# Kernel optimization log

Measured on AMD Instinct MI355X. Metric: run time of the kernel, lower is better.

Reference implementation:

```python
import jax, jax.numpy as jnp
import numpy as np

N_HEADS = 16
KEY_DIM = 64
VAL_DIM = 64
HIDDEN = 1024
SCALE = 1.0 / float(KEY_DIM) ** 0.5


def setup_inputs() -> dict:
    key = jax.random.key(0)
    ks = jax.random.split(key, 16)
    B, Lq, Lk, R = 2, 2048, 2048, 2048
    inp = {
        "query": jax.random.normal(ks[0], (B, Lq, HIDDEN), jnp.float32),
        "value": jax.random.normal(ks[1], (B, Lk, HIDDEN), jnp.float32),
        "positional_embedding": jax.random.normal(ks[2], (R, HIDDEN), jnp.float32),
        "u_weight": jax.random.normal(ks[3], (N_HEADS, KEY_DIM), jnp.float32) * 0.02,
        "v_weight": jax.random.normal(ks[4], (N_HEADS, KEY_DIM), jnp.float32) * 0.02,
        "indices": jax.random.randint(ks[5], (2, Lq, Lk), 0, R, jnp.int64 if jax.config.jax_enable_x64 else jnp.int32),
        "lower": jax.random.uniform(ks[6], (Lq, Lk), jnp.float32),
    }
    s = 0.02
    inp["Wq"] = jax.random.normal(ks[7], (HIDDEN, N_HEADS * KEY_DIM), jnp.float32) * s
    inp["bq"] = jnp.zeros((N_HEADS * KEY_DIM,), jnp.float32)
    inp["Wk"] = jax.random.normal(ks[8], (HIDDEN, N_HEADS * KEY_DIM), jnp.float32) * s
    inp["bk"] = jnp.zeros((N_HEADS * KEY_DIM,), jnp.float32)
    inp["Wv"] = jax.random.normal(ks[9], (HIDDEN, N_HEADS * VAL_DIM), jnp.float32) * s
    inp["bv"] = jnp.zeros((N_HEADS * VAL_DIM,), jnp.float32)
    inp["Wr"] = jax.random.normal(ks[10], (HIDDEN, N_HEADS * KEY_DIM), jnp.float32) * s
    inp["br"] = jnp.zeros((N_HEADS * KEY_DIM,), jnp.float32)
    inp["Wo"] = jax.random.normal(ks[11], (N_HEADS * VAL_DIM, HIDDEN), jnp.float32) * s
    inp["bo"] = jnp.zeros((HIDDEN,), jnp.float32)
    return inp


def reference(query, value, positional_embedding, u_weight, v_weight, indices, lower,
              Wq, bq, Wk, bk, Wv, bv, Wr, br, Wo, bo):
    B, Lq, _ = query.shape
    Lk = value.shape[1]
    R = positional_embedding.shape[0]
    # projections (torch Linear with weights stored as [in, out])
    q = (query @ Wq + bq).reshape(B, Lq, N_HEADS, KEY_DIM)
    k = (value @ Wk + bk).reshape(B, Lk, N_HEADS, KEY_DIM)
    v = (value @ Wv + bv).reshape(B, Lk, N_HEADS, VAL_DIM)
    r = (positional_embedding @ Wr + br).reshape(R, N_HEADS, KEY_DIM)
    # content (AC) and position (BD) score terms -> [i, j, b, n]
    AC = jnp.einsum("bind,bjnd->ijbn", q + u_weight, k)
    BD = jnp.einsum("bind,jnd->ijbn", q + v_weight, r)
    # rel-shift: gather [Lq, R] -> [Lq, Lk] positions, then apply lower mask
    BD = BD[indices[0], indices[1]] * lower[:, :, None, None]
    attn = jax.nn.softmax((AC + BD) * SCALE, axis=1)  # softmax over key dim j
    out = jnp.einsum("ijbn,bjnd->bind", attn, v).reshape(B, Lq, N_HEADS * VAL_DIM)
    return out @ Wo + bo
```

## Files before the change

kernel.cpp:

```cpp
#include <hip/hip_runtime.h>
#include <stdint.h>

typedef __attribute__((ext_vector_type(8))) short short8;
typedef __attribute__((ext_vector_type(4))) float f32x4;
typedef unsigned short u16;
typedef unsigned int u32;
typedef unsigned long long u64;

#define LQ 2048
#define LK 2048
#define RDIM 2048
#define HID 1024
#define NH 16
#define DH 64
#define S2SCALE 0.1803368801111204f

__device__ __forceinline__ float bf2f(u16 u){
  union { unsigned int i; float f; } v; v.i = ((unsigned int)u) << 16; return v.f;
}
__device__ __forceinline__ u16 f2bf(float f){
  union { float f; unsigned int i; } v; v.f = f;
  unsigned int r = v.i + 0x7fffu + ((v.i >> 16) & 1u);
  return (u16)(r >> 16);
}
__device__ __forceinline__ f32x4 fzero(){ f32x4 z = {0.0f, 0.0f, 0.0f, 0.0f}; return z; }

__global__ void k_detect(const u32* __restrict__ q, const u32* __restrict__ idxw,
                         int* __restrict__ flags){
  int t = threadIdx.x;
  u32 w = q[t];
  int b = (w >> 7) & 0xFF;
  unsigned long long mb = __ballot(b >= 100 && b <= 140);
  u32 hi = idxw[2 * t + 1];
  unsigned long long mi = __ballot(hi == 0u);
  if (t == 0){
    flags[0] = (__popcll(mb) >= 48) ? 1 : 0;
    flags[1] = (__popcll(mi) == 64) ? 1 : 0;
  }
}

struct Seg { const void* src; u16* dst; int n4; };
struct SegPack { Seg s[8]; };
__global__ void k_ingestN(SegPack p, const int* __restrict__ flags){
  int f = flags[0];
  Seg sg = p.s[blockIdx.y];
  int stride = gridDim.x * blockDim.x;
  for (int i = blockIdx.x * blockDim.x + threadIdx.x; i < sg.n4; i += stride){
    if (f){
      reinterpret_cast<uint2*>(sg.dst)[i] = reinterpret_cast<const uint2*>(sg.src)[i];
    } else {
      float4 v = reinterpret_cast<const float4*>(sg.src)[i];
      union { u16 h[4]; uint2 u; } t;
      t.h[0] = f2bf(v.x); t.h[1] = f2bf(v.y); t.h[2] = f2bf(v.z); t.h[3] = f2bf(v.w);
      reinterpret_cast<uint2*>(sg.dst)[i] = t.u;
    }
  }
}

struct WPack { const void* src[5]; u16* dst[5]; };
__global__ void k_wtrans(WPack p, const int* __restrict__ flags){
  int f = flags[0];
  const void* W = p.src[blockIdx.z];
  u16* Wt = p.dst[blockIdx.z];
  __shared__ u16 t[64][65];
  int tid = threadIdx.x;
  int bx = blockIdx.x, by = blockIdx.y;
#pragma unroll
  for (int it = 0; it < 16; ++it){
    int id = it * 256 + tid;
    int r = id >> 6, c = id & 63;
    size_t so = (size_t)(by * 64 + r) * HID + bx * 64 + c;
    t[r][c] = f ? ((const u16*)W)[so] : f2bf(((const float*)W)[so]);
  }
  __syncthreads();
#pragma unroll
  for (int it = 0; it < 16; ++it){
    int id = it * 256 + tid;
    int r = id >> 6, c = id & 63;
    Wt[(size_t)(bx * 64 + r) * HID + by * 64 + c] = t[c][r];
  }
}

__global__ void k_goff(const int* __restrict__ idx, int* __restrict__ goff,
                       const int* __restrict__ flags){
  int i64f = flags[1];
  const size_t N = (size_t)LQ * LK;
  size_t stride = (size_t)gridDim.x * blockDim.x;
  for (size_t t = (size_t)blockIdx.x * blockDim.x + threadIdx.x; t < N; t += stride){
    long long a0, a1;
    if (i64f){
      const long long* ip = (const long long*)idx;
      a0 = ip[t]; a1 = ip[N + t];
    } else {
      a0 = idx[t]; a1 = idx[N + t];
    }
    goff[t] = (int)(a0 * RDIM + a1);
  }
}

__global__ void k_gemm(const u16* __restrict__ A, const u16* __restrict__ Bt,
                       const u16* __restrict__ bias,
                       const u16* __restrict__ add0, const u16* __restrict__ add1,
                       void* __restrict__ D0, u16* __restrict__ D1,
                       int headmajor, const int* __restrict__ oflags){
  __shared__ u16 As[128][72];
  __shared__ u16 Bs[128][72];
  int tid = threadIdx.x;
  int l = tid & 63, w = tid >> 6;
  int lr = l & 15, g = l >> 4;
  int wr = w >> 1, wc = w & 1;
  int outf32 = oflags ? (oflags[0] == 0) : 0;
  f32x4 acc[4][4];
#pragma unroll
  for (int a = 0; a < 4; ++a)
#pragma unroll
    for (int bq_ = 0; bq_ < 4; ++bq_) acc[a][bq_] = fzero();
  const size_t arowg = (size_t)blockIdx.x * 128;
  const size_t browg = (size_t)blockIdx.y * 128;
  for (int kt = 0; kt < HID; kt += 64){
#pragma unroll
    for (int it = 0; it < 4; ++it){
      int id = it * 256 + tid;
      int r = id >> 3, ch = id & 7;
      uint4 va = *reinterpret_cast<const uint4*>(A + (arowg + r) * HID + kt + ch * 8);
      *reinterpret_cast<uint4*>(&As[r][ch * 8]) = va;
      uint4 vb = *reinterpret_cast<const uint4*>(Bt + (browg + r) * HID + kt + ch * 8);
      *reinterpret_cast<uint4*>(&Bs[r][ch * 8]) = vb;
    }
    __syncthreads();
#pragma unroll
    for (int ks = 0; ks < 2; ++ks){
      short8 af[4], bfv[4];
#pragma unroll
      for (int mf = 0; mf < 4; ++mf)
        af[mf] = *reinterpret_cast<const short8*>(&As[wr * 64 + mf * 16 + lr][ks * 32 + 8 * g]);
#pragma unroll
      for (int nf = 0; nf < 4; ++nf)
        bfv[nf] = *reinterpret_cast<const short8*>(&Bs[wc * 64 + nf * 16 + lr][ks * 32 + 8 * g]);
#pragma unroll
      for (int mf = 0; mf < 4; ++mf)
#pragma unroll
        for (int nf = 0; nf < 4; ++nf)
          acc[mf][nf] = __builtin_amdgcn_mfma_f32_16x16x32_bf16(af[mf], bfv[nf], acc[mf][nf], 0, 0, 0);
    }
    __syncthreads();
  }
#pragma unroll
  for (int mf = 0; mf < 4; ++mf)
#pragma unroll
    for (int nf = 0; nf < 4; ++nf){
      int col = (int)browg + wc * 64 + nf * 16 + lr;
      float bcol = bf2f(bias[col]);
      float a0 = add0 ? bf2f(add0[col]) : 0.0f;
      float a1 = add1 ? bf2f(add1[col]) : 0.0f;
#pragma unroll
      for (int reg = 0; reg < 4; ++reg){
        int row = (int)arowg + wr * 64 + mf * 16 + 4 * g + reg;
        float base = acc[mf][nf][reg] + bcol;
        if (headmajor == 2){
          int b = row >> 11, i = row & 2047;
          int n32 = col >> 6, d = col & 63;
          u16* Dx = (n32 < NH) ? (u16*)D0 : D1;
          size_t dst = ((size_t)(b * NH + (n32 & (NH - 1))) * LQ + i) * DH + d;
          Dx[dst] = f2bf(base);
        } else if (headmajor == 1){
          int b = row >> 11, i = row & 2047;
          int n = col >> 6, d = col & 63;
          size_t dst = ((size_t)(b * NH + n) * LQ + i) * DH + d;
          ((u16*)D0)[dst] = f2bf(base + a0);
          if (D1) D1[dst] = f2bf(base + a1);
        } else {
          size_t dst = (size_t)row * HID + col;
          if (outf32) ((float*)D0)[dst] = base;
          else        ((u16*)D0)[dst] = f2bf(base);
        }
      }
    }
}

__global__ void k_bdfull16(const u16* __restrict__ qv, const u16* __restrict__ rr,
                           u16* __restrict__ bdf, int bnBase){
  __shared__ u16 tile[32][64][16];
  int tid = threadIdx.x;
  int l = tid & 63, w = tid >> 6;
  int lr = l & 15, g = l >> 4;
  int i0 = blockIdx.x * 32, j0 = blockIdx.y * 64;
#pragma unroll
  for (int hh = 0; hh < 4; ++hh){
    int g_ = w * 4 + hh;
    int bn = bnBase + g_;
    int b = bn >> 4, n = bn & 15;
    const u16* qb = qv + ((size_t)(b * NH + n) * LQ + i0) * DH;
    const u16* rb = rr + ((size_t)n * RDIM + j0) * DH;
    short8 af[2][2];
#pragma unroll
    for (int mf = 0; mf < 2; ++mf)
#pragma unroll
      for (int ks = 0; ks < 2; ++ks)
        af[mf][ks] = *reinterpret_cast<const short8*>(qb + (size_t)(mf * 16 + lr) * DH + ks * 32 + 8 * g);
    f32x4 acc[2][4];
#pragma unroll
    for (int mf = 0; mf < 2; ++mf)
#pragma unroll
      for (int nf = 0; nf < 4; ++nf) acc[mf][nf] = fzero();
#pragma unroll
    for (int nf = 0; nf < 4; ++nf){
#pragma unroll
      for (int ks = 0; ks < 2; ++ks){
        short8 bb = *reinterpret_cast<const short8*>(rb + (size_t)(nf * 16 + lr) * DH + ks * 32 + 8 * g);
#pragma unroll
        for (int mf = 0; mf < 2; ++mf)
          acc[mf][nf] = __builtin_amdgcn_mfma_f32_16x16x32_bf16(af[mf][ks], bb, acc[mf][nf], 0, 0, 0);
      }
    }
#pragma unroll
    for (int mf = 0; mf < 2; ++mf)
#pragma unroll
      for (int nf = 0; nf < 4; ++nf)
#pragma unroll
        for (int reg = 0; reg < 4; ++reg)
          tile[mf * 16 + 4 * g + reg][nf * 16 + lr][g_] = f2bf(acc[mf][nf][reg]);
  }
  __syncthreads();
#pragma unroll
  for (int e = 0; e < 32; ++e){
    int id = e * 256 + tid;
    int line = id >> 2, part = id & 3;
    int ii = line >> 6, jj = line & 63;
    u64 v = *reinterpret_cast<const u64*>(&tile[ii][jj][part * 4]);
    *reinterpret_cast<u64*>(
        bdf + ((size_t)(i0 + ii) * RDIM + (size_t)(j0 + jj)) * 16 + part * 4) = v;
  }
}

__global__ void k_bdfull8(const u16* __restrict__ qv, const u16* __restrict__ rr,
                          u16* __restrict__ bdf, int bnBase){
  __shared__ u16 tile[32][64][8];
  int tid = threadIdx.x;
  int l = tid & 63, w = tid >> 6;
  int lr = l & 15, g = l >> 4;
  int i0 = blockIdx.x * 32, j0 = blockIdx.y * 64;
#pragma unroll
  for (int hh = 0; hh < 2; ++hh){
    int g_ = w * 2 + hh;
    int bn = bnBase + g_;
    int b = bn >> 4, n = bn & 15;
    const u16* qb = qv + ((size_t)(b * NH + n) * LQ + i0) * DH;
    const u16* rb = rr + ((size_t)n * RDIM + j0) * DH;
    short8 af[2][2];
#pragma unroll
    for (int mf = 0; mf < 2; ++mf)
#pragma unroll
      for (int ks = 0; ks < 2; ++ks)
        af[mf][ks] = *reinterpret_cast<const short8*>(qb + (size_t)(mf * 16 + lr) * DH + ks * 32 + 8 * g);
    f32x4 acc[2][4];
#pragma unroll
    for (int mf = 0; mf < 2; ++mf)
#pragma unroll
      for (int nf = 0; nf < 4; ++nf) acc[mf][nf] = fzero();
#pragma unroll
    for (int nf = 0; nf < 4; ++nf){
#pragma unroll
      for (int ks = 0; ks < 2; ++ks){
        short8 bb = *reinterpret_cast<const short8*>(rb + (size_t)(nf * 16 + lr) * DH + ks * 32 + 8 * g);
#pragma unroll
        for (int mf = 0; mf < 2; ++mf)
          acc[mf][nf] = __builtin_amdgcn_mfma_f32_16x16x32_bf16(af[mf][ks], bb, acc[mf][nf], 0, 0, 0);
      }
    }
#pragma unroll
    for (int mf = 0; mf < 2; ++mf)
#pragma unroll
      for (int nf = 0; nf < 4; ++nf)
#pragma unroll
        for (int reg = 0; reg < 4; ++reg)
          tile[mf * 16 + 4 * g + reg][nf * 16 + lr][g_] = f2bf(acc[mf][nf][reg]);
  }
  __syncthreads();
#pragma unroll
  for (int e = 0; e < 16; ++e){
    int id = e * 256 + tid;
    int line = id >> 1, part = id & 1;
    int ii = line >> 6, jj = line & 63;
    u64 v = *reinterpret_cast<const u64*>(&tile[ii][jj][part * 4]);
    *reinterpret_cast<u64*>(
        bdf + ((size_t)(i0 + ii) * RDIM + (size_t)(j0 + jj)) * 8 + part * 4) = v;
  }
}

template<int G>
__global__ void k_bdfull(const u16* __restrict__ qv, const u16* __restrict__ rr,
                         u16* __restrict__ bdf, int bnBase){
  __shared__ u16 tile[16][32][G];
  int tid = threadIdx.x;
  int l = tid & 63, w = tid >> 6;
  int lr = l & 15, g = l >> 4;
  int i0 = blockIdx.x * 16, j0 = blockIdx.y * 32;
  if (w < G){
    int g_ = w;
    int bn = bnBase + g_;
    int b = bn >> 4, n = bn & 15;
    const u16* qb = qv + ((size_t)(b * NH + n) * LQ + i0) * DH;
    const u16* rb = rr + ((size_t)n * RDIM + j0) * DH;
    f32x4 acc2[2];
    acc2[0] = fzero(); acc2[1] = fzero();
#pragma unroll
    for (int ks = 0; ks < 2; ++ks){
      short8 a = *reinterpret_cast<const short8*>(qb + (size_t)lr * DH + ks * 32 + 8 * g);
#pragma unroll
      for (int nf = 0; nf < 2; ++nf){
        short8 bb = *reinterpret_cast<const short8*>(rb + (size_t)(lr + 16 * nf) * DH + ks * 32 + 8 * g);
        acc2[nf] = __builtin_amdgcn_mfma_f32_16x16x32_bf16(a, bb, acc2[nf], 0, 0, 0);
      }
    }
#pragma unroll
    for (int nf = 0; nf < 2; ++nf){
      int jj = lr + 16 * nf;
#pragma unroll
      for (int reg = 0; reg < 4; ++reg)
        tile[4 * g + reg][jj][g_] = f2bf(acc2[nf][reg]);
    }
  }
  __syncthreads();
  constexpr int CHUNKS = 512;
#pragma unroll
  for (int e = 0; e < (CHUNKS * G + 255) / 256 && e * 256 < CHUNKS * G; ++e){
    int id = e * 256 + tid;
    if (id >= CHUNKS * G) break;
    int line = id / G, k = id % G;
    int ii = line >> 5, jj = line & 31;
    bdf[((size_t)(i0 + ii) * RDIM + (size_t)(j0 + jj)) * G + k] = tile[ii][jj][k];
  }
}

template<int G>
__global__ void k_gather(const u16* __restrict__ bdf, const int* __restrict__ goff,
                         const u16* __restrict__ lower, u16* __restrict__ bdg){
  __shared__ u16 tile[G][16][32];
  int tid = threadIdx.x;
  int i0 = blockIdx.x * 16, j0 = blockIdx.y * 32;
#pragma unroll
  for (int it = 0; it < 2; ++it){
    int p = it * 256 + tid;
    int ii = p >> 5, jj = p & 31;
    size_t off = (size_t)(i0 + ii) * LK + (j0 + jj);
    int go = goff[off];
    float lw = bf2f(lower[off]);
    const u16* src = bdf + (size_t)go * G;
    union { uint4 q[2]; u32 w2[8]; u16 h[16]; } uv;
    if (G == 16){
      uv.q[0] = *reinterpret_cast<const uint4*>(src);
      uv.q[1] = *reinterpret_cast<const uint4*>(src + 8);
    } else if (G == 8){
      uv.q[0] = *reinterpret_cast<const uint4*>(src);
    } else if (G == 2){
      uv.w2[0] = *reinterpret_cast<const u32*>(src);
    } else {
      uv.h[0] = *src;
    }
#pragma unroll
    for (int k = 0; k < G; ++k)
      tile[k][ii][jj] = f2bf(bf2f(uv.h[k]) * lw);
  }
  __syncthreads();
  constexpr int CHUNKS = G * 128;
#pragma unroll
  for (int e = 0; e < (CHUNKS + 255) / 256; ++e){
    int id = e * 256 + tid;
    if (CHUNKS < 256 * ((CHUNKS + 255) / 256) && id >= CHUNKS) break;
    int g_ = id >> 7, rem = id & 127;
    int ii = rem >> 3, part = rem & 7;
    u64 v = *reinterpret_cast<const u64*>(&tile[g_][ii][part * 4]);
    __builtin_nontemporal_store(v, reinterpret_cast<u64*>(
        bdg + (size_t)g_ * LQ * LK + (size_t)(i0 + ii) * LK + j0 + part * 4));
  }
}

__device__ __forceinline__ void flash_compute(
    int lr, int g,
    const short8& aq0, const short8& aq1,
    f32x4* O, float* mrun, float* lacc,
    u16 (*klds)[72], u16 (*vtlds)[128], u16 (*pldsw)[136]){
  float sv[8][4];
#pragma unroll
  for (int nf = 0; nf < 8; ++nf){
    f32x4 z = fzero();
    short8 bk0 = *reinterpret_cast<const short8*>(&klds[lr + 16 * nf][8 * g]);
    short8 bk1 = *reinterpret_cast<const short8*>(&klds[lr + 16 * nf][32 + 8 * g]);
    z = __builtin_amdgcn_mfma_f32_16x16x32_bf16(aq0, bk0, z, 0, 0, 0);
    z = __builtin_amdgcn_mfma_f32_16x16x32_bf16(aq1, bk1, z, 0, 0, 0);
#pragma unroll
    for (int reg = 0; reg < 4; ++reg){
      float bd = bf2f(pldsw[4 * g + reg][lr + 16 * nf]);
      sv[nf][reg] = (z[reg] + bd) * S2SCALE;
    }
  }
  float fs[4];
#pragma unroll
  for (int reg = 0; reg < 4; ++reg){
    float mx = sv[0][reg];
#pragma unroll
    for (int nf = 1; nf < 8; ++nf) mx = fmaxf(mx, sv[nf][reg]);
#pragma unroll
    for (int d = 1; d < 16; d <<= 1) mx = fmaxf(mx, __shfl_xor(mx, d));
    float mnew = fmaxf(mrun[reg], mx);
    fs[reg] = exp2f(mrun[reg] - mnew);
    mrun[reg] = mnew;
    float sumloc = 0.0f;
#pragma unroll
    for (int nf = 0; nf < 8; ++nf){
      sv[nf][reg] = exp2f(sv[nf][reg] - mnew);
      sumloc += sv[nf][reg];
    }
    lacc[reg] = lacc[reg] * fs[reg] + sumloc;
  }
#pragma unroll
  for (int nf = 0; nf < 4; ++nf)
#pragma unroll
    for (int reg = 0; reg < 4; ++reg)
      O[nf][reg] *= fs[reg];
#pragma unroll
  for (int nf = 0; nf < 8; ++nf)
#pragma unroll
    for (int reg = 0; reg < 4; ++reg)
      pldsw[4 * g + reg][lr + 16 * nf] = f2bf(sv[nf][reg]);
  short8 pa[4];
#pragma unroll
  for (int ks = 0; ks < 4; ++ks)
    pa[ks] = *reinterpret_cast<const short8*>(&pldsw[lr][ks * 32 + 8 * g]);
#pragma unroll
  for (int nf = 0; nf < 4; ++nf){
    int d = lr + 16 * nf;
#pragma unroll
    for (int ks = 0; ks < 4; ++ks){
      int cv = ((ks * 4 + g) ^ (d >> 3)) * 8;
      short8 bv = *reinterpret_cast<const short8*>(&vtlds[d][cv]);
      O[nf] = __builtin_amdgcn_mfma_f32_16x16x32_bf16(pa[ks], bv, O[nf], 0, 0, 0);
    }
  }
}

__global__ __launch_bounds__(256) void k_flash(
    const u16* __restrict__ qu, const u16* __restrict__ kk,
    const u16* __restrict__ vv, const u16* __restrict__ bdg,
    u16* __restrict__ oo, int bnBase){
  __shared__ u16 klds[128][72];
  __shared__ u16 vtlds[64][128];
  __shared__ u16 plds[4][16][136];
  int tid = threadIdx.x;
  int l = tid & 63, w = tid >> 6;
  int lr = l & 15, g = l >> 4;
  int gi = blockIdx.x;
  int bn = bnBase + gi;
  int b = bn >> 4, n = bn & 15;
  int i0 = blockIdx.y * 64;
  const u16* qb = qu + ((size_t)bn * LQ + i0 + w * 16) * DH;
  short8 aq0 = *reinterpret_cast<const short8*>(qb + (size_t)lr * DH + 8 * g);
  short8 aq1 = *reinterpret_cast<const short8*>(qb + (size_t)lr * DH + 32 + 8 * g);
  f32x4 O[4];
#pragma unroll
  for (int nf = 0; nf < 4; ++nf) O[nf] = fzero();
  float mrun[4], lacc[4];
#pragma unroll
  for (int r = 0; r < 4; ++r){ mrun[r] = -1e30f; lacc[r] = 0.0f; }
  const u16* kbase = kk + (size_t)bn * LK * DH;
  const u16* vbase = vv + (size_t)bn * LK * DH;
  const u16* bdw = bdg + (size_t)gi * LQ * LK + (size_t)(i0 + w * 16) * LK;
  u16 (*pldsw)[136] = plds[w];
  int brow = l >> 2, bq = l & 3;

  uint4 kv[8];
  uint4 bdv[4];

#define LOADALL(J_) do { _Pragma("unroll") for (int it_ = 0; it_ < 4; ++it_){ \
    int id_ = it_ * 256 + tid; int r_ = id_ >> 3, ch_ = id_ & 7; \
    kv[it_]     = *reinterpret_cast<const uint4*>(kbase + (size_t)((J_) + r_) * DH + ch_ * 8); \
    kv[4 + it_] = *reinterpret_cast<const uint4*>(vbase + (size_t)((J_) + r_) * DH + ch_ * 8); } \
    _Pragma("unroll") for (int c_ = 0; c_ < 4; ++c_) \
      bdv[c_] = *reinterpret_cast<const uint4*>(bdw + (size_t)brow * LK + (J_) + (c_ * 4 + bq) * 8); } while(0)

#define WRITEALL() do { _Pragma("unroll") for (int it_ = 0; it_ < 4; ++it_){ \
    int id_ = it_ * 256 + tid; int r_ = id_ >> 3, ch_ = id_ & 7; \
    *reinterpret_cast<uint4*>(&klds[r_][ch_ * 8]) = kv[it_]; \
    u16 tmp_[8]; *reinterpret_cast<uint4*>(tmp_) = kv[4 + it_]; \
    int cb_ = r_ ^ (ch_ * 8); \
    _Pragma("unroll") for (int e_ = 0; e_ < 8; ++e_) vtlds[ch_ * 8 + e_][cb_] = tmp_[e_]; } \
    _Pragma("unroll") for (int c_ = 0; c_ < 4; ++c_) \
      *reinterpret_cast<uint4*>(&pldsw[brow][(c_ * 4 + bq) * 8]) = bdv[c_]; } while(0)

  LOADALL(0);
  WRITEALL();
  __syncthreads();

  for (int t = 0; t < 16; ++t){
    if (t < 15) LOADALL((t + 1) * 128);
    flash_compute(lr, g, aq0, aq1, O, mrun, lacc, klds, vtlds, pldsw);
    if (t < 15){
      __syncthreads();
      WRITEALL();
      __syncthreads();
    }
  }
#undef LOADALL
#undef WRITEALL

  float lsum[4];
#pragma unroll
  for (int reg = 0; reg < 4; ++reg){
    float s = lacc[reg];
#pragma unroll
    for (int d = 1; d < 16; d <<= 1) s += __shfl_xor(s, d);
    lsum[reg] = s;
  }
#pragma unroll
  for (int nf = 0; nf < 4; ++nf)
#pragma unroll
    for (int reg = 0; reg < 4; ++reg){
      int i = i0 + w * 16 + 4 * g + reg;
      float vo = O[nf][reg] / lsum[reg];
      oo[((size_t)(b * LQ + i)) * HID + n * DH + lr + 16 * nf] = f2bf(vo);
    }
}

extern "C" void kernel_launch(void* const* d_in, const int* in_sizes, int n_in,
                              void* d_out, int out_size, void* d_ws, size_t ws_size,
                              hipStream_t stream){
  const void* query = d_in[0];
  const void* value = d_in[1];
  const void* pos   = d_in[2];
  const void* uw    = d_in[3];
  const void* vw    = d_in[4];
  const int* idx    = (const int*)d_in[5];
  const void* lower = d_in[6];
  const void* Wq = d_in[7];  const void* bq = d_in[8];
  const void* Wk = d_in[9];  const void* bk = d_in[10];
  const void* Wv = d_in[11]; const void* bv = d_in[12];
  const void* Wr = d_in[13]; const void* br = d_in[14];
  const void* Wo = d_in[15]; const void* bo = d_in[16];
  (void)in_sizes; (void)n_in; (void)out_size;

  char* ws = (char*)d_ws;
  const size_t MB = (size_t)1 << 20;
  u16* cquery = (u16*)(ws + 0 * MB);
  u16* cvalue = (u16*)(ws + 8 * MB);
  int* goff   = (int*)(ws + 0 * MB);
  u16* cpos   = (u16*)(ws + 16 * MB);
  u16* clower = (u16*)(ws + 20 * MB);
  char* sm = ws + 28 * MB;
  u16* cuw = (u16*)(sm + 0 * 4096);
  u16* cvw = (u16*)(sm + 1 * 4096);
  u16* cbq = (u16*)(sm + 2 * 4096);
  u16* cbk = (u16*)(sm + 3 * 4096);
  u16* cbv = cbk + 1024;
  u16* cbr = (u16*)(sm + 5 * 4096);
  u16* cbo = (u16*)(sm + 6 * 4096);
  int* flags = (int*)(sm + 7 * 4096);
  u16* wot = (u16*)(ws + 29 * MB);
  u16* wqt = (u16*)(ws + 31 * MB);
  u16* wkt = (u16*)(ws + 33 * MB);
  u16* wvt = (u16*)(ws + 35 * MB);
  u16* wrt = (u16*)(ws + 37 * MB);
  u16* qu  = (u16*)(ws + 39 * MB);
  u16* qv  = (u16*)(ws + 47 * MB);
  u16* kkp = (u16*)(ws + 55 * MB);
  u16* vvp = (u16*)(ws + 63 * MB);
  u16* rrp = (u16*)(ws + 71 * MB);
  u16* oo  = (u16*)(ws + 75 * MB);
  u16* bdf = (u16*)(ws + 84 * MB);

  dim3 blk(256);
  k_detect<<<1, 64, 0, stream>>>((const u32*)query, (const u32*)idx, flags);

  {
    SegPack big;
    big.s[0] = { query, cquery, 2 * LQ * HID / 4 };
    big.s[1] = { value, cvalue, 2 * LK * HID / 4 };
    big.s[2] = { pos,   cpos,   RDIM * HID / 4 };
    big.s[3] = { lower, clower, LQ * LK / 4 };
    for (int i = 4; i < 8; ++i) big.s[i] = { nullptr, nullptr, 0 };
    k_ingestN<<<dim3(512, 4), blk, 0, stream>>>(big, flags);
    SegPack sml;
    sml.s[0] = { uw, cuw, NH * DH / 4 };
    sml.s[1] = { vw, cvw, NH * DH / 4 };
    sml.s[2] = { bq, cbq, HID / 4 };
    sml.s[3] = { bk, cbk, HID / 4 };
    sml.s[4] = { bv, cbv, HID / 4 };
    sml.s[5] = { br, cbr, HID / 4 };
    sml.s[6] = { bo, cbo, HID / 4 };
    sml.s[7] = { nullptr, nullptr, 0 };
    k_ingestN<<<dim3(4, 7), blk, 0, stream>>>(sml, flags);
  }
  {
    WPack wp;
    wp.src[0] = Wq; wp.dst[0] = wqt;
    wp.src[1] = Wk; wp.dst[1] = wkt;
    wp.src[2] = Wv; wp.dst[2] = wvt;
    wp.src[3] = Wr; wp.dst[3] = wrt;
    wp.src[4] = Wo; wp.dst[4] = wot;
    k_wtrans<<<dim3(16, 16, 5), blk, 0, stream>>>(wp, flags);
  }

  k_gemm<<<dim3(32, 8), blk, 0, stream>>>(cquery, wqt, cbq, cuw, cvw, qu, qv, 1, nullptr);
  k_gemm<<<dim3(32, 16), blk, 0, stream>>>(cvalue, wkt, cbk, nullptr, nullptr, kkp, vvp, 2, nullptr);
  k_gemm<<<dim3(16, 8), blk, 0, stream>>>(cpos, wrt, cbr, nullptr, nullptr, rrp, nullptr, 1, nullptr);

  k_goff<<<dim3(1024), blk, 0, stream>>>(idx, goff, flags);

  if (ws_size >= 340 * MB){
    u16* bdg = (u16*)(ws + 212 * MB);
    for (int b0 = 0; b0 < 2 * NH; b0 += 16){
      k_bdfull16<<<dim3(64, 32), blk, 0, stream>>>(qv, rrp, bdf, b0);
      k_gather<16><<<dim3(128, 64), blk, 0, stream>>>(bdf, goff, clower, bdg);
      k_flash<<<dim3(16, 32), blk, 0, stream>>>(qu, kkp, vvp, bdg, oo, b0);
    }
  } else if (ws_size >= 212 * MB){
    u16* bdg = (u16*)(ws + 148 * MB);
    for (int b0 = 0; b0 < 2 * NH; b0 += 8){
      k_bdfull8<<<dim3(64, 32), blk, 0, stream>>>(qv, rrp, bdf, b0);
      k_gather<8><<<dim3(128, 64), blk, 0, stream>>>(bdf, goff, clower, bdg);
      k_flash<<<dim3(8, 32), blk, 0, stream>>>(qu, kkp, vvp, bdg, oo, b0);
    }
  } else if (ws_size >= 116 * MB){
    u16* bdg = (u16*)(ws + 100 * MB);
    for (int b0 = 0; b0 < 2 * NH; b0 += 2){
      k_bdfull<2><<<dim3(128, 64), blk, 0, stream>>>(qv, rrp, bdf, b0);
      k_gather<2><<<dim3(128, 64), blk, 0, stream>>>(bdf, goff, clower, bdg);
      k_flash<<<dim3(2, 32), blk, 0, stream>>>(qu, kkp, vvp, bdg, oo, b0);
    }
  } else {
    u16* bdg = (u16*)(ws + 92 * MB);
    for (int b0 = 0; b0 < 2 * NH; b0 += 1){
      k_bdfull<1><<<dim3(128, 64), blk, 0, stream>>>(qv, rrp, bdf, b0);
      k_gather<1><<<dim3(128, 64), blk, 0, stream>>>(bdf, goff, clower, bdg);
      k_flash<<<dim3(1, 32), blk, 0, stream>>>(qu, kkp, vvp, bdg, oo, b0);
    }
  }
  k_gemm<<<dim3(32, 8), blk, 0, stream>>>(oo, wot, cbo, nullptr, nullptr, d_out, nullptr, 0, flags);
}
```

Measured before the change: 995.4 us.

## Split gather/flash into query-row halves and pad V-transpose LDS rows

The gathered BD buffer for 16 heads is now produced and consumed in two halves of 1024 query rows each. This halves its footprint, so the 16-head path works with a smaller workspace threshold and the intermediate is more likely to stay in the last-level cache between gather and flash. The V-transpose LDS tile is padded from 128 to 136 columns to reduce bank conflicts. The cost is twice as many kernel launches, with smaller grids (256 flash blocks per launch).

After: 979.9 us. Within noise of the previous version (-1.6%).

```diff
diff --git a/kernel.cpp b/kernel.cpp
--- a/kernel.cpp
+++ b/kernel.cpp
@@ -335,10 +335,11 @@
 
 template<int G>
 __global__ void k_gather(const u16* __restrict__ bdf, const int* __restrict__ goff,
-                         const u16* __restrict__ lower, u16* __restrict__ bdg){
+                         const u16* __restrict__ lower, u16* __restrict__ bdg,
+                         int iBase, int iSpan){
   __shared__ u16 tile[G][16][32];
   int tid = threadIdx.x;
-  int i0 = blockIdx.x * 16, j0 = blockIdx.y * 32;
+  int i0 = iBase + blockIdx.x * 16, j0 = blockIdx.y * 32;
 #pragma unroll
   for (int it = 0; it < 2; ++it){
     int p = it * 256 + tid;
@@ -372,7 +373,7 @@
     int ii = rem >> 3, part = rem & 7;
     u64 v = *reinterpret_cast<const u64*>(&tile[g_][ii][part * 4]);
     __builtin_nontemporal_store(v, reinterpret_cast<u64*>(
-        bdg + (size_t)g_ * LQ * LK + (size_t)(i0 + ii) * LK + j0 + part * 4));
+        bdg + (size_t)g_ * iSpan * LK + (size_t)(i0 - iBase + ii) * LK + j0 + part * 4));
   }
 }
 
@@ -380,7 +381,7 @@
     int lr, int g,
     const short8& aq0, const short8& aq1,
     f32x4* O, float* mrun, float* lacc,
-    u16 (*klds)[72], u16 (*vtlds)[128], u16 (*pldsw)[136]){
+    u16 (*klds)[72], u16 (*vtlds)[136], u16 (*pldsw)[136]){
   float sv[8][4];
 #pragma unroll
   for (int nf = 0; nf < 8; ++nf){
@@ -443,9 +444,9 @@
 __global__ __launch_bounds__(256) void k_flash(
     const u16* __restrict__ qu, const u16* __restrict__ kk,
     const u16* __restrict__ vv, const u16* __restrict__ bdg,
-    u16* __restrict__ oo, int bnBase){
+    u16* __restrict__ oo, int bnBase, int iBase, int iSpan){
   __shared__ u16 klds[128][72];
-  __shared__ u16 vtlds[64][128];
+  __shared__ u16 vtlds[64][136];
   __shared__ u16 plds[4][16][136];
   int tid = threadIdx.x;
   int l = tid & 63, w = tid >> 6;
@@ -453,7 +454,7 @@
   int gi = blockIdx.x;
   int bn = bnBase + gi;
   int b = bn >> 4, n = bn & 15;
-  int i0 = blockIdx.y * 64;
+  int i0 = iBase + blockIdx.y * 64;
   const u16* qb = qu + ((size_t)bn * LQ + i0 + w * 16) * DH;
   short8 aq0 = *reinterpret_cast<const short8*>(qb + (size_t)lr * DH + 8 * g);
   short8 aq1 = *reinterpret_cast<const short8*>(qb + (size_t)lr * DH + 32 + 8 * g);
@@ -465,7 +466,7 @@
   for (int r = 0; r < 4; ++r){ mrun[r] = -1e30f; lacc[r] = 0.0f; }
   const u16* kbase = kk + (size_t)bn * LK * DH;
   const u16* vbase = vv + (size_t)bn * LK * DH;
-  const u16* bdw = bdg + (size_t)gi * LQ * LK + (size_t)(i0 + w * 16) * LK;
+  const u16* bdw = bdg + (size_t)gi * iSpan * LK + (size_t)(i0 - iBase + w * 16) * LK;
   u16 (*pldsw)[136] = plds[w];
   int brow = l >> 2, bq = l & 3;
 
@@ -606,33 +607,35 @@
 
   k_goff<<<dim3(1024), blk, 0, stream>>>(idx, goff, flags);
 
-  if (ws_size >= 340 * MB){
+  if (ws_size >= 276 * MB){
     u16* bdg = (u16*)(ws + 212 * MB);
     for (int b0 = 0; b0 < 2 * NH; b0 += 16){
       k_bdfull16<<<dim3(64, 32), blk, 0, stream>>>(qv, rrp, bdf, b0);
-      k_gather<16><<<dim3(128, 64), blk, 0, stream>>>(bdf, goff, clower, bdg);
-      k_flash<<<dim3(16, 32), blk, 0, stream>>>(qu, kkp, vvp, bdg, oo, b0);
+      for (int ih = 0; ih < LQ; ih += 1024){
+        k_gather<16><<<dim3(64, 64), blk, 0, stream>>>(bdf, goff, clower, bdg, ih, 1024);
+        k_flash<<<dim3(16, 16), blk, 0, stream>>>(qu, kkp, vvp, bdg, oo, b0, ih, 1024);
+      }
     }
   } else if (ws_size >= 212 * MB){
     u16* bdg = (u16*)(ws + 148 * MB);
     for (int b0 = 0; b0 < 2 * NH; b0 += 8){
       k_bdfull8<<<dim3(64, 32), blk, 0, stream>>>(qv, rrp, bdf, b0);
-      k_gather<8><<<dim3(128, 64), blk, 0, stream>>>(bdf, goff, clower, bdg);
-      k_flash<<<dim3(8, 32), blk, 0, stream>>>(qu, kkp, vvp, bdg, oo, b0);
+      k_gather<8><<<dim3(128, 64), blk, 0, stream>>>(bdf, goff, clower, bdg, 0, LQ);
+      k_flash<<<dim3(8, 32), blk, 0, stream>>>(qu, kkp, vvp, bdg, oo, b0, 0, LQ);
     }
   } else if (ws_size >= 116 * MB){
     u16* bdg = (u16*)(ws + 100 * MB);
     for (int b0 = 0; b0 < 2 * NH; b0 += 2){
       k_bdfull<2><<<dim3(128, 64), blk, 0, stream>>>(qv, rrp, bdf, b0);
-      k_gather<2><<<dim3(128, 64), blk, 0, stream>>>(bdf, goff, clower, bdg);
-      k_flash<<<dim3(2, 32), blk, 0, stream>>>(qu, kkp, vvp, bdg, oo, b0);
+      k_gather<2><<<dim3(128, 64), blk, 0, stream>>>(bdf, goff, clower, bdg, 0, LQ);
+      k_flash<<<dim3(2, 32), blk, 0, stream>>>(qu, kkp, vvp, bdg, oo, b0, 0, LQ);
     }
   } else {
     u16* bdg = (u16*)(ws + 92 * MB);
     for (int b0 = 0; b0 < 2 * NH; b0 += 1){
       k_bdfull<1><<<dim3(128, 64), blk, 0, stream>>>(qv, rrp, bdf, b0);
-      k_gather<1><<<dim3(128, 64), blk, 0, stream>>>(bdf, goff, clower, bdg);
-      k_flash<<<dim3(1, 32), blk, 0, stream>>>(qu, kkp, vvp, bdg, oo, b0);
+      k_gather<1><<<dim3(128, 64), blk, 0, stream>>>(bdf, goff, clower, bdg, 0, LQ);
+      k_flash<<<dim3(1, 32), blk, 0, stream>>>(qu, kkp, vvp, bdg, oo, b0, 0, LQ);
     }
   }
   k_gemm<<<dim3(32, 8), blk, 0, stream>>>(oo, wot, cbo, nullptr, nullptr, d_out, nullptr, 0, flags);
```

## Split flash attention key range across two wave groups with final merge

Applied to the files above, without the earlier changes.

The flash kernel now runs 512 threads per block. Two halves of four waves each process alternating 128-key chunks for the same 64 query rows. At the end they merge their partial outputs, running maxima and sums through shared memory with rescaling. This doubles the parallelism per block and halves the serial key loop. It also drops the 16-head batching path, so large workspaces now fall into the 8-head path, and the V-transpose LDS row is padded to 136. The cost is more LDS, a merge step, and the loss of the 16-way batching.

Measured after the change: 977.8 us. No clear change (-1.8%).

```diff
diff --git a/kernel.cpp b/kernel.cpp
--- a/kernel.cpp
+++ b/kernel.cpp
@@ -178,61 +178,6 @@
     }
 }
 
-__global__ void k_bdfull16(const u16* __restrict__ qv, const u16* __restrict__ rr,
-                           u16* __restrict__ bdf, int bnBase){
-  __shared__ u16 tile[32][64][16];
-  int tid = threadIdx.x;
-  int l = tid & 63, w = tid >> 6;
-  int lr = l & 15, g = l >> 4;
-  int i0 = blockIdx.x * 32, j0 = blockIdx.y * 64;
-#pragma unroll
-  for (int hh = 0; hh < 4; ++hh){
-    int g_ = w * 4 + hh;
-    int bn = bnBase + g_;
-    int b = bn >> 4, n = bn & 15;
-    const u16* qb = qv + ((size_t)(b * NH + n) * LQ + i0) * DH;
-    const u16* rb = rr + ((size_t)n * RDIM + j0) * DH;
-    short8 af[2][2];
-#pragma unroll
-    for (int mf = 0; mf < 2; ++mf)
-#pragma unroll
-      for (int ks = 0; ks < 2; ++ks)
-        af[mf][ks] = *reinterpret_cast<const short8*>(qb + (size_t)(mf * 16 + lr) * DH + ks * 32 + 8 * g);
-    f32x4 acc[2][4];
-#pragma unroll
-    for (int mf = 0; mf < 2; ++mf)
-#pragma unroll
-      for (int nf = 0; nf < 4; ++nf) acc[mf][nf] = fzero();
-#pragma unroll
-    for (int nf = 0; nf < 4; ++nf){
-#pragma unroll
-      for (int ks = 0; ks < 2; ++ks){
-        short8 bb = *reinterpret_cast<const short8*>(rb + (size_t)(nf * 16 + lr) * DH + ks * 32 + 8 * g);
-#pragma unroll
-        for (int mf = 0; mf < 2; ++mf)
-          acc[mf][nf] = __builtin_amdgcn_mfma_f32_16x16x32_bf16(af[mf][ks], bb, acc[mf][nf], 0, 0, 0);
-      }
-    }
-#pragma unroll
-    for (int mf = 0; mf < 2; ++mf)
-#pragma unroll
-      for (int nf = 0; nf < 4; ++nf)
-#pragma unroll
-        for (int reg = 0; reg < 4; ++reg)
-          tile[mf * 16 + 4 * g + reg][nf * 16 + lr][g_] = f2bf(acc[mf][nf][reg]);
-  }
-  __syncthreads();
-#pragma unroll
-  for (int e = 0; e < 32; ++e){
-    int id = e * 256 + tid;
-    int line = id >> 2, part = id & 3;
-    int ii = line >> 6, jj = line & 63;
-    u64 v = *reinterpret_cast<const u64*>(&tile[ii][jj][part * 4]);
-    *reinterpret_cast<u64*>(
-        bdf + ((size_t)(i0 + ii) * RDIM + (size_t)(j0 + jj)) * 16 + part * 4) = v;
-  }
-}
-
 __global__ void k_bdfull8(const u16* __restrict__ qv, const u16* __restrict__ rr,
                           u16* __restrict__ bdf, int bnBase){
   __shared__ u16 tile[32][64][8];
@@ -380,7 +325,7 @@
     int lr, int g,
     const short8& aq0, const short8& aq1,
     f32x4* O, float* mrun, float* lacc,
-    u16 (*klds)[72], u16 (*vtlds)[128], u16 (*pldsw)[136]){
+    u16 (*klds)[72], u16 (*vtlds)[136], u16 (*pldsw)[136]){
   float sv[8][4];
 #pragma unroll
   for (int nf = 0; nf < 8; ++nf){
@@ -440,21 +385,24 @@
   }
 }
 
-__global__ __launch_bounds__(256) void k_flash(
+__global__ __launch_bounds__(512) void k_flash(
     const u16* __restrict__ qu, const u16* __restrict__ kk,
     const u16* __restrict__ vv, const u16* __restrict__ bdg,
     u16* __restrict__ oo, int bnBase){
-  __shared__ u16 klds[128][72];
-  __shared__ u16 vtlds[64][128];
-  __shared__ u16 plds[4][16][136];
+  __shared__ u16 klds[2][128][72];
+  __shared__ u16 vtlds[2][64][136];
+  __shared__ u16 plds[2][4][16][136];
+  __shared__ float exch[4][16][68];
   int tid = threadIdx.x;
   int l = tid & 63, w = tid >> 6;
   int lr = l & 15, g = l >> 4;
+  int half = w >> 2, wl = w & 3;
+  int tid_h = tid & 255;
   int gi = blockIdx.x;
   int bn = bnBase + gi;
   int b = bn >> 4, n = bn & 15;
   int i0 = blockIdx.y * 64;
-  const u16* qb = qu + ((size_t)bn * LQ + i0 + w * 16) * DH;
+  const u16* qb = qu + ((size_t)bn * LQ + i0 + wl * 16) * DH;
   short8 aq0 = *reinterpret_cast<const short8*>(qb + (size_t)lr * DH + 8 * g);
   short8 aq1 = *reinterpret_cast<const short8*>(qb + (size_t)lr * DH + 32 + 8 * g);
   f32x4 O[4];
@@ -465,37 +413,41 @@
   for (int r = 0; r < 4; ++r){ mrun[r] = -1e30f; lacc[r] = 0.0f; }
   const u16* kbase = kk + (size_t)bn * LK * DH;
   const u16* vbase = vv + (size_t)bn * LK * DH;
-  const u16* bdw = bdg + (size_t)gi * LQ * LK + (size_t)(i0 + w * 16) * LK;
-  u16 (*pldsw)[136] = plds[w];
+  const u16* bdw = bdg + (size_t)gi * LQ * LK + (size_t)(i0 + wl * 16) * LK;
+  u16 (*kldsh)[72] = klds[half];
+  u16 (*vtldsh)[136] = vtlds[half];
+  u16 (*pldsw)[136] = plds[half][wl];
   int brow = l >> 2, bq = l & 3;
 
   uint4 kv[8];
   uint4 bdv[4];
 
 #define LOADALL(J_) do { _Pragma("unroll") for (int it_ = 0; it_ < 4; ++it_){ \
-    int id_ = it_ * 256 + tid; int r_ = id_ >> 3, ch_ = id_ & 7; \
+    int id_ = it_ * 256 + tid_h; int r_ = id_ >> 3, ch_ = id_ & 7; \
     kv[it_]     = *reinterpret_cast<const uint4*>(kbase + (size_t)((J_) + r_) * DH + ch_ * 8); \
     kv[4 + it_] = *reinterpret_cast<const uint4*>(vbase + (size_t)((J_) + r_) * DH + ch_ * 8); } \
     _Pragma("unroll") for (int c_ = 0; c_ < 4; ++c_) \
       bdv[c_] = *reinterpret_cast<const uint4*>(bdw + (size_t)brow * LK + (J_) + (c_ * 4 + bq) * 8); } while(0)
 
 #define WRITEALL() do { _Pragma("unroll") for (int it_ = 0; it_ < 4; ++it_){ \
-    int id_ = it_ * 256 + tid; int r_ = id_ >> 3, ch_ = id_ & 7; \
-    *reinterpret_cast<uint4*>(&klds[r_][ch_ * 8]) = kv[it_]; \
+    int id_ = it_ * 256 + tid_h; int r_ = id_ >> 3, ch_ = id_ & 7; \
+    *reinterpret_cast<uint4*>(&kldsh[r_][ch_ * 8]) = kv[it_]; \
     u16 tmp_[8]; *reinterpret_cast<uint4*>(tmp_) = kv[4 + it_]; \
     int cb_ = r_ ^ (ch_ * 8); \
-    _Pragma("unroll") for (int e_ = 0; e_ < 8; ++e_) vtlds[ch_ * 8 + e_][cb_] = tmp_[e_]; } \
+    _Pragma("unroll") for (int e_ = 0; e_ < 8; ++e_) vtldsh[ch_ * 8 + e_][cb_] = tmp_[e_]; } \
     _Pragma("unroll") for (int c_ = 0; c_ < 4; ++c_) \
       *reinterpret_cast<uint4*>(&pldsw[brow][(c_ * 4 + bq) * 8]) = bdv[c_]; } while(0)
 
-  LOADALL(0);
+  int jcur = half * 128;
+  LOADALL(jcur);
   WRITEALL();
   __syncthreads();
 
-  for (int t = 0; t < 16; ++t){
-    if (t < 15) LOADALL((t + 1) * 128);
-    flash_compute(lr, g, aq0, aq1, O, mrun, lacc, klds, vtlds, pldsw);
-    if (t < 15){
+  for (int t = 0; t < 8; ++t){
+    int jnext = (t + 1) * 256 + half * 128;
+    if (t < 7) LOADALL(jnext);
+    flash_compute(lr, g, aq0, aq1, O, mrun, lacc, kldsh, vtldsh, pldsw);
+    if (t < 7){
       __syncthreads();
       WRITEALL();
       __syncthreads();
@@ -512,14 +464,41 @@
     for (int d = 1; d < 16; d <<= 1) s += __shfl_xor(s, d);
     lsum[reg] = s;
   }
-#pragma unroll
-  for (int nf = 0; nf < 4; ++nf)
+  __syncthreads();
+  if (half == 1){
+#pragma unroll
+    for (int nf = 0; nf < 4; ++nf)
+#pragma unroll
+      for (int reg = 0; reg < 4; ++reg)
+        exch[wl][4 * g + reg][lr + 16 * nf] = O[nf][reg];
+    if (lr == 0){
+#pragma unroll
+      for (int reg = 0; reg < 4; ++reg){
+        exch[wl][4 * g + reg][64] = mrun[reg];
+        exch[wl][4 * g + reg][65] = lsum[reg];
+      }
+    }
+  }
+  __syncthreads();
+  if (half == 0){
 #pragma unroll
     for (int reg = 0; reg < 4; ++reg){
-      int i = i0 + w * 16 + 4 * g + reg;
-      float vo = O[nf][reg] / lsum[reg];
-      oo[((size_t)(b * LQ + i)) * HID + n * DH + lr + 16 * nf] = f2bf(vo);
-    }
+      int rrow = 4 * g + reg;
+      float mB = exch[wl][rrow][64];
+      float lB = exch[wl][rrow][65];
+      float m = fmaxf(mrun[reg], mB);
+      float sA = exp2f(mrun[reg] - m);
+      float sB = exp2f(mB - m);
+      float denom = lsum[reg] * sA + lB * sB;
+      int i = i0 + wl * 16 + rrow;
+#pragma unroll
+      for (int nf = 0; nf < 4; ++nf){
+        float ob = exch[wl][rrow][lr + 16 * nf];
+        float vo = (O[nf][reg] * sA + ob * sB) / denom;
+        oo[((size_t)(b * LQ + i)) * HID + n * DH + lr + 16 * nf] = f2bf(vo);
+      }
+    }
+  }
 }
 
 extern "C" void kernel_launch(void* const* d_in, const int* in_sizes, int n_in,
@@ -606,33 +585,26 @@
 
   k_goff<<<dim3(1024), blk, 0, stream>>>(idx, goff, flags);
 
-  if (ws_size >= 340 * MB){
-    u16* bdg = (u16*)(ws + 212 * MB);
-    for (int b0 = 0; b0 < 2 * NH; b0 += 16){
-      k_bdfull16<<<dim3(64, 32), blk, 0, stream>>>(qv, rrp, bdf, b0);
-      k_gather<16><<<dim3(128, 64), blk, 0, stream>>>(bdf, goff, clower, bdg);
-      k_flash<<<dim3(16, 32), blk, 0, stream>>>(qu, kkp, vvp, bdg, oo, b0);
-    }
-  } else if (ws_size >= 212 * MB){
+  if (ws_size >= 212 * MB){
     u16* bdg = (u16*)(ws + 148 * MB);
     for (int b0 = 0; b0 < 2 * NH; b0 += 8){
       k_bdfull8<<<dim3(64, 32), blk, 0, stream>>>(qv, rrp, bdf, b0);
       k_gather<8><<<dim3(128, 64), blk, 0, stream>>>(bdf, goff, clower, bdg);
-      k_flash<<<dim3(8, 32), blk, 0, stream>>>(qu, kkp, vvp, bdg, oo, b0);
+      k_flash<<<dim3(8, 32), dim3(512), 0, stream>>>(qu, kkp, vvp, bdg, oo, b0);
     }
   } else if (ws_size >= 116 * MB){
     u16* bdg = (u16*)(ws + 100 * MB);
     for (int b0 = 0; b0 < 2 * NH; b0 += 2){
       k_bdfull<2><<<dim3(128, 64), blk, 0, stream>>>(qv, rrp, bdf, b0);
       k_gather<2><<<dim3(128, 64), blk, 0, stream>>>(bdf, goff, clower, bdg);
-      k_flash<<<dim3(2, 32), blk, 0, stream>>>(qu, kkp, vvp, bdg, oo, b0);
+      k_flash<<<dim3(2, 32), dim3(512), 0, stream>>>(qu, kkp, vvp, bdg, oo, b0);
     }
   } else {
     u16* bdg = (u16*)(ws + 92 * MB);
     for (int b0 = 0; b0 < 2 * NH; b0 += 1){
       k_bdfull<1><<<dim3(128, 64), blk, 0, stream>>>(qv, rrp, bdf, b0);
       k_gather<1><<<dim3(128, 64), blk, 0, stream>>>(bdf, goff, clower, bdg);
-      k_flash<<<dim3(1, 32), blk, 0, stream>>>(qu, kkp, vvp, bdg, oo, b0);
+      k_flash<<<dim3(1, 32), dim3(512), 0, stream>>>(qu, kkp, vvp, bdg, oo, b0);
     }
   }
   k_gemm<<<dim3(32, 8), blk, 0, stream>>>(oo, wot, cbo, nullptr, nullptr, d_out, nullptr, 0, flags);
```
